# Kernel optimization log

Measured on AMD Instinct MI355X. Metric: run time of the kernel, lower is better.

## Reference

```python
import jax, jax.numpy as jnp
import numpy as np

B, CTX, QST, E, H = 8, 4096, 512, 300, 128

def setup_inputs() -> dict:
    key = jax.random.key(0)
    k1, k2, k3, k4 = jax.random.split(key, 4)
    context_sequence = jax.random.normal(k1, (B, CTX, E), dtype=jnp.float32)
    question_sequence = jax.random.normal(k2, (B, QST, E), dtype=jnp.float32)
    question_mask = jnp.ones((B, QST), dtype=jnp.int32)
    # dense layer params (PyTorch Linear: y = x @ W.T + b)
    bound = 1.0 / np.sqrt(E)
    W = jax.random.uniform(k3, (H, E), minval=-bound, maxval=bound, dtype=jnp.float32)
    b = jax.random.uniform(k4, (H,), minval=-bound, maxval=bound, dtype=jnp.float32)
    return {"context_sequence": context_sequence, "question_sequence": question_sequence,
            "question_mask": question_mask, "W": W, "b": b}

def reference(context_sequence, question_sequence, question_mask, W, b):
    # ReLU(dense(x)) for both sequences
    ctx_logits = jax.nn.relu(jnp.einsum('bce,he->bch', context_sequence, W) + b)   # [B, CTX, H]
    qst_logits = jax.nn.relu(jnp.einsum('bqe,he->bqh', question_sequence, W) + b)  # [B, QST, H]
    scores = jnp.einsum('bch,bqh->bcq', ctx_logits, qst_logits)                    # [B, CTX, QST]
    scores = jnp.where(question_mask[:, None, :] == 0, -jnp.inf, scores)
    attn = jax.nn.softmax(scores, axis=-1)
    return jnp.einsum('bcq,bqh->bch', attn, qst_logits)                            # [B, CTX, H]
```

## Files before the change

### kernel.cpp

```cpp
#include <hip/hip_runtime.h>
#include <hip/hip_bf16.h>

#define BB   8
#define SCTX 4096
#define SQ   512
#define EE   300
#define HH   128
#define EP   320
#define CST  328
#define LOG2E 1.4426950408889634f

typedef short short8 __attribute__((ext_vector_type(8)));
typedef float f32x4  __attribute__((ext_vector_type(4)));

#define MFMA16(a, b, c) __builtin_amdgcn_mfma_f32_16x16x32_bf16((a), (b), (c), 0, 0, 0)

__device__ __forceinline__ short f2bf(float f) {
  unsigned u = __builtin_bit_cast(unsigned, f);
  u += 0x7fffu + ((u >> 16) & 1u);
  return (short)(u >> 16);
}

__global__ void k_wpad(const float* __restrict__ W, short* __restrict__ wpad) {
  const int h = blockIdx.x, k = threadIdx.x;
  float v = (k < EE) ? W[h * EE + k] : 0.0f;
  wpad[h * EP + k] = f2bf(v);
}

__global__ __launch_bounds__(256) void k_qlog(const float* __restrict__ qst,
                                              const short* __restrict__ wpad,
                                              const float* __restrict__ bias,
                                              short* __restrict__ ql,
                                              short* __restrict__ qlT) {
  const int b = blockIdx.y;
  const int m0 = blockIdx.x * 32;
  const int tid = threadIdx.x;
  const int w = tid >> 6, l = tid & 63, t = l & 15, quad = l >> 4;
  const int g = w >> 1, hf = w & 1;

  __shared__ __align__(16) short cst[32 * CST];

  const float4* cbase = (const float4*)(qst + (size_t)(b * SQ + m0) * EE);
#pragma unroll
  for (int j = 0; j < 10; ++j) {
    int i4 = tid + j * 256;
    if (i4 < 2400) {
      float4 v = cbase[i4];
      int row = i4 / 75, c4 = i4 - row * 75;
      short* dp = cst + row * CST + c4 * 4;
      dp[0] = f2bf(v.x); dp[1] = f2bf(v.y); dp[2] = f2bf(v.z); dp[3] = f2bf(v.w);
    }
  }
  for (int i = tid; i < 320; i += 256) {
    int row = i / 10, c = (i - row * 10) * 2;
    cst[row * CST + 300 + c] = 0;
    cst[row * CST + 301 + c] = 0;
  }
  __syncthreads();

  const short* arow = cst + (g * 16 + t) * CST;
  f32x4 acc[4] = {};
#pragma unroll
  for (int kk = 0; kk < 10; ++kk) {
    const int k = kk * 32 + quad * 8;
    short8 a = *(const short8*)(arow + k);
#pragma unroll
    for (int n = 0; n < 4; ++n) {
      short8 w8 = *(const short8*)(wpad + ((hf * 4 + n) * 16 + t) * EP + k);
      acc[n] = MFMA16(a, w8, acc[n]);
    }
  }
#pragma unroll
  for (int n = 0; n < 4; ++n) {
    const int h = (hf * 4 + n) * 16 + t;
    const float bv = bias[h];
#pragma unroll
    for (int r = 0; r < 4; ++r) {
      float v = fmaxf(acc[n][r] + bv, 0.0f);
      short s16 = f2bf(v);
      const int row = m0 + g * 16 + quad * 4 + r;
      ql[((size_t)b * SQ + row) * HH + h] = s16;
      qlT[((size_t)b * HH + h) * SQ + row] = s16;
    }
  }
}

__global__ __launch_bounds__(256, 2) void k_attn(const float* __restrict__ ctx,
                                                 const short* __restrict__ wpad,
                                                 const float* __restrict__ bias,
                                                 const int* __restrict__ mask,
                                                 const short* __restrict__ ql,
                                                 const short* __restrict__ qlT,
                                                 float* __restrict__ out) {
  const int b = blockIdx.y;
  const int m0 = blockIdx.x * 64;
  const int tid = threadIdx.x;
  const int w = tid >> 6, l = tid & 63, t = l & 15, quad = l >> 4;
  const int g = w >> 1, hf = w & 1;

  __shared__ __align__(16) short uq[17408];
  __shared__ __align__(16) short uc[8704];
  __shared__ float maskb[SQ];
  short* cst = uq;
  short* qch = uq;
  short* clt = uc;
  short* pbw = uc + w * 2176;

  for (int i = tid; i < SQ; i += 256)
    maskb[i] = mask[b * SQ + i] ? 0.0f : -1e30f;

  for (int i = 0; i < 2; ++i) {
    const float4* cbase = (const float4*)(ctx + ((size_t)b * SCTX + m0 + i * 32) * EE);
#pragma unroll
    for (int j = 0; j < 10; ++j) {
      int i4 = tid + j * 256;
      if (i4 < 2400) {
        float4 v = cbase[i4];
        int row = i4 / 75, c4 = i4 - row * 75;
        short* dp = cst + row * CST + c4 * 4;
        dp[0] = f2bf(v.x); dp[1] = f2bf(v.y); dp[2] = f2bf(v.z); dp[3] = f2bf(v.w);
      }
    }
    for (int k = tid; k < 320; k += 256) {
      int row = k / 10, c = (k - row * 10) * 2;
      cst[row * CST + 300 + c] = 0;
      cst[row * CST + 301 + c] = 0;
    }
    __syncthreads();
    const short* arow = cst + (g * 16 + t) * CST;
    f32x4 acc[4] = {};
#pragma unroll
    for (int kk = 0; kk < 10; ++kk) {
      const int k = kk * 32 + quad * 8;
      short8 a = *(const short8*)(arow + k);
#pragma unroll
      for (int n = 0; n < 4; ++n) {
        short8 w8 = *(const short8*)(wpad + ((hf * 4 + n) * 16 + t) * EP + k);
        acc[n] = MFMA16(a, w8, acc[n]);
      }
    }
#pragma unroll
    for (int n = 0; n < 4; ++n) {
      const int h = (hf * 4 + n) * 16 + t;
      const float bv = bias[h];
#pragma unroll
      for (int r = 0; r < 4; ++r) {
        float v = fmaxf(acc[n][r] + bv, 0.0f);
        clt[(i * 32 + g * 16 + quad * 4 + r) * 136 + h] = f2bf(v);
      }
    }
    __syncthreads();
  }

  short8 af[4];
#pragma unroll
  for (int kk = 0; kk < 4; ++kk)
    af[kk] = *(const short8*)&clt[(w * 16 + t) * 136 + kk * 32 + quad * 8];

  f32x4 s[32];
  const short8* qsrc = (const short8*)(ql + (size_t)b * SQ * HH);
  short8 ld[8];
#pragma unroll
  for (int j = 0; j < 8; ++j) ld[j] = qsrc[tid + j * 256];
#pragma unroll
  for (int c = 0; c < 4; ++c) {
    if (c) __syncthreads();
#pragma unroll
    for (int j = 0; j < 8; ++j) {
      int i = tid + j * 256;
      int row = i >> 4, c16 = i & 15;
      *(short8*)&qch[row * 136 + c16 * 8] = ld[j];
    }
    __syncthreads();
    if (c < 3) {
#pragma unroll
      for (int j = 0; j < 8; ++j) ld[j] = qsrc[(c + 1) * 2048 + tid + j * 256];
    }
#pragma unroll
    for (int n2 = 0; n2 < 8; ++n2) {
      f32x4 sv = {0.f, 0.f, 0.f, 0.f};
      const short* qrow = qch + (n2 * 16 + t) * 136;
#pragma unroll
      for (int kk = 0; kk < 4; ++kk) {
        short8 b8 = *(const short8*)(qrow + kk * 32 + quad * 8);
        sv = MFMA16(af[kk], b8, sv);
      }
      s[c * 8 + n2] = sv;
    }
  }

#pragma unroll
  for (int n = 0; n < 32; ++n) {
    const float mb = maskb[(n >> 3) * 128 + (n & 7) * 16 + t];
    s[n][0] += mb; s[n][1] += mb; s[n][2] += mb; s[n][3] += mb;
  }
  f32x4 rmax = s[0];
#pragma unroll
  for (int n = 1; n < 32; ++n)
#pragma unroll
    for (int r = 0; r < 4; ++r) rmax[r] = fmaxf(rmax[r], s[n][r]);
#pragma unroll
  for (int off = 8; off; off >>= 1)
#pragma unroll
    for (int r = 0; r < 4; ++r) rmax[r] = fmaxf(rmax[r], __shfl_xor(rmax[r], off));
  f32x4 rsum = {0.f, 0.f, 0.f, 0.f};
#pragma unroll
  for (int n = 0; n < 32; ++n)
#pragma unroll
    for (int r = 0; r < 4; ++r) {
      float p = exp2f((s[n][r] - rmax[r]) * LOG2E);
      s[n][r] = p;
      rsum[r] += p;
    }
#pragma unroll
  for (int off = 8; off; off >>= 1)
#pragma unroll
    for (int r = 0; r < 4; ++r) rsum[r] += __shfl_xor(rsum[r], off);

  const short8* vsrc = (const short8*)(qlT + (size_t)b * HH * SQ);
#pragma unroll
  for (int j = 0; j < 8; ++j) {
    int i = tid + j * 256;
    ld[j] = vsrc[(i >> 4) * 64 + (i & 15)];
  }
  f32x4 o[8] = {};
#pragma unroll
  for (int c = 0; c < 4; ++c) {
    __syncthreads();
#pragma unroll
    for (int j = 0; j < 8; ++j) {
      int i = tid + j * 256;
      int row = i >> 4, c16 = i & 15;
      *(short8*)&qch[row * 136 + c16 * 8] = ld[j];
    }
#pragma unroll
    for (int n2 = 0; n2 < 8; ++n2)
#pragma unroll
      for (int r = 0; r < 4; ++r)
        pbw[(quad * 4 + r) * 136 + n2 * 16 + t] = f2bf(s[c * 8 + n2][r]);
    __syncthreads();
    if (c < 3) {
#pragma unroll
      for (int j = 0; j < 8; ++j) {
        int i = tid + j * 256;
        ld[j] = vsrc[(i >> 4) * 64 + (c + 1) * 16 + (i & 15)];
      }
    }
#pragma unroll
    for (int kk = 0; kk < 4; ++kk) {
      short8 pa = *(const short8*)&pbw[t * 136 + kk * 32 + quad * 8];
#pragma unroll
      for (int n = 0; n < 8; ++n) {
        short8 v8 = *(const short8*)&qch[(n * 16 + t) * 136 + kk * 32 + quad * 8];
        o[n] = MFMA16(pa, v8, o[n]);
      }
    }
  }

  f32x4 rinv;
#pragma unroll
  for (int r = 0; r < 4; ++r) rinv[r] = 1.0f / rsum[r];
  float* obase = out + ((size_t)b * SCTX + m0 + w * 16) * HH;
#pragma unroll
  for (int n = 0; n < 8; ++n)
#pragma unroll
    for (int r = 0; r < 4; ++r)
      obase[(quad * 4 + r) * HH + n * 16 + t] = o[n][r] * rinv[r];
}

extern "C" void kernel_launch(void* const* d_in, const int* in_sizes, int n_in,
                              void* d_out, int out_size, void* d_ws, size_t ws_size,
                              hipStream_t stream) {
  const float* ctx  = (const float*)d_in[0];
  const float* qst  = (const float*)d_in[1];
  const int*   mask = (const int*)d_in[2];
  const float* W    = (const float*)d_in[3];
  const float* bias = (const float*)d_in[4];
  float* out = (float*)d_out;

  short* wpad = (short*)d_ws;
  short* ql   = (short*)((char*)d_ws + 81920);
  short* qlT  = ql + (size_t)BB * SQ * HH;

  k_wpad<<<dim3(HH), dim3(EP), 0, stream>>>(W, wpad);
  k_qlog<<<dim3(SQ / 32, BB), dim3(256), 0, stream>>>(qst, wpad, bias, ql, qlT);
  k_attn<<<dim3(SCTX / 64, BB), dim3(256), 0, stream>>>(ctx, wpad, bias, mask, ql, qlT, out);
}
```

Before: 130.5 us.

## Use online softmax per chunk, swizzle W for coalesced MFMA loads, raise occupancy

The attention kernel now keeps a running max and sum per chunk of 128 questions instead of holding all 32 score tiles in registers, so register pressure drops and launch bounds go to 3 blocks per SU. The weight matrix is pre-swizzled into MFMA fragment order, so each lane reads a contiguous 16 bytes. The register prefetch of the next Q/V chunk is removed, which exposes global load latency at each chunk. It also adds a rescale of the output accumulators per chunk.

```diff
diff --git a/kernel.cpp b/kernel.cpp
--- a/kernel.cpp
+++ b/kernel.cpp
@@ -21,14 +21,15 @@
   return (short)(u >> 16);
 }
 
-__global__ void k_wpad(const float* __restrict__ W, short* __restrict__ wpad) {
+__global__ void k_wpad(const float* __restrict__ W, short* __restrict__ wsw) {
   const int h = blockIdx.x, k = threadIdx.x;
   float v = (k < EE) ? W[h * EE + k] : 0.0f;
-  wpad[h * EP + k] = f2bf(v);
+  const int m = h >> 4, t = h & 15, kk = k >> 5, quad = (k >> 3) & 3, j = k & 7;
+  wsw[((kk * 8 + m) * 64 + quad * 16 + t) * 8 + j] = f2bf(v);
 }
 
 __global__ __launch_bounds__(256) void k_qlog(const float* __restrict__ qst,
-                                              const short* __restrict__ wpad,
+                                              const short* __restrict__ wsw,
                                               const float* __restrict__ bias,
                                               short* __restrict__ ql,
                                               short* __restrict__ qlT) {
@@ -66,7 +67,7 @@
     short8 a = *(const short8*)(arow + k);
 #pragma unroll
     for (int n = 0; n < 4; ++n) {
-      short8 w8 = *(const short8*)(wpad + ((hf * 4 + n) * 16 + t) * EP + k);
+      short8 w8 = *(const short8*)(wsw + ((kk * 8 + hf * 4 + n) * 64 + l) * 8);
       acc[n] = MFMA16(a, w8, acc[n]);
     }
   }
@@ -85,8 +86,8 @@
   }
 }
 
-__global__ __launch_bounds__(256, 2) void k_attn(const float* __restrict__ ctx,
-                                                 const short* __restrict__ wpad,
+__global__ __launch_bounds__(256, 3) void k_attn(const float* __restrict__ ctx,
+                                                 const short* __restrict__ wsw,
                                                  const float* __restrict__ bias,
                                                  const int* __restrict__ mask,
                                                  const short* __restrict__ ql,
@@ -135,7 +136,7 @@
       short8 a = *(const short8*)(arow + k);
 #pragma unroll
       for (int n = 0; n < 4; ++n) {
-        short8 w8 = *(const short8*)(wpad + ((hf * 4 + n) * 16 + t) * EP + k);
+        short8 w8 = *(const short8*)(wsw + ((kk * 8 + hf * 4 + n) * 64 + l) * 8);
         acc[n] = MFMA16(a, w8, acc[n]);
       }
     }
@@ -157,25 +158,25 @@
   for (int kk = 0; kk < 4; ++kk)
     af[kk] = *(const short8*)&clt[(w * 16 + t) * 136 + kk * 32 + quad * 8];
 
-  f32x4 s[32];
   const short8* qsrc = (const short8*)(ql + (size_t)b * SQ * HH);
-  short8 ld[8];
-#pragma unroll
-  for (int j = 0; j < 8; ++j) ld[j] = qsrc[tid + j * 256];
-#pragma unroll
+  const short8* vsrc = (const short8*)(qlT + (size_t)b * HH * SQ);
+
+  f32x4 o[8] = {};
+  f32x4 m_run, l_run;
+#pragma unroll
+  for (int r = 0; r < 4; ++r) { m_run[r] = -3.0e38f; l_run[r] = 0.0f; }
+
   for (int c = 0; c < 4; ++c) {
     if (c) __syncthreads();
 #pragma unroll
     for (int j = 0; j < 8; ++j) {
       int i = tid + j * 256;
-      int row = i >> 4, c16 = i & 15;
-      *(short8*)&qch[row * 136 + c16 * 8] = ld[j];
-    }
-    __syncthreads();
-    if (c < 3) {
-#pragma unroll
-      for (int j = 0; j < 8; ++j) ld[j] = qsrc[(c + 1) * 2048 + tid + j * 256];
-    }
+      short8 v = qsrc[c * 2048 + i];
+      *(short8*)&qch[(i >> 4) * 136 + (i & 15) * 8] = v;
+    }
+    __syncthreads();
+
+    f32x4 s[8];
 #pragma unroll
     for (int n2 = 0; n2 < 8; ++n2) {
       f32x4 sv = {0.f, 0.f, 0.f, 0.f};
@@ -185,67 +186,61 @@
         short8 b8 = *(const short8*)(qrow + kk * 32 + quad * 8);
         sv = MFMA16(af[kk], b8, sv);
       }
-      s[c * 8 + n2] = sv;
-    }
-  }
-
-#pragma unroll
-  for (int n = 0; n < 32; ++n) {
-    const float mb = maskb[(n >> 3) * 128 + (n & 7) * 16 + t];
-    s[n][0] += mb; s[n][1] += mb; s[n][2] += mb; s[n][3] += mb;
-  }
-  f32x4 rmax = s[0];
-#pragma unroll
-  for (int n = 1; n < 32; ++n)
-#pragma unroll
-    for (int r = 0; r < 4; ++r) rmax[r] = fmaxf(rmax[r], s[n][r]);
-#pragma unroll
-  for (int off = 8; off; off >>= 1)
-#pragma unroll
-    for (int r = 0; r < 4; ++r) rmax[r] = fmaxf(rmax[r], __shfl_xor(rmax[r], off));
-  f32x4 rsum = {0.f, 0.f, 0.f, 0.f};
-#pragma unroll
-  for (int n = 0; n < 32; ++n)
+      const float mb = maskb[c * 128 + n2 * 16 + t];
+      sv[0] += mb; sv[1] += mb; sv[2] += mb; sv[3] += mb;
+      s[n2] = sv;
+    }
+
+    f32x4 cm = s[0];
+#pragma unroll
+    for (int n2 = 1; n2 < 8; ++n2)
+#pragma unroll
+      for (int r = 0; r < 4; ++r) cm[r] = fmaxf(cm[r], s[n2][r]);
+#pragma unroll
+    for (int off = 8; off; off >>= 1)
+#pragma unroll
+      for (int r = 0; r < 4; ++r) cm[r] = fmaxf(cm[r], __shfl_xor(cm[r], off));
+
+    f32x4 alpha, csum = {0.f, 0.f, 0.f, 0.f};
 #pragma unroll
     for (int r = 0; r < 4; ++r) {
-      float p = exp2f((s[n][r] - rmax[r]) * LOG2E);
-      s[n][r] = p;
-      rsum[r] += p;
-    }
-#pragma unroll
-  for (int off = 8; off; off >>= 1)
-#pragma unroll
-    for (int r = 0; r < 4; ++r) rsum[r] += __shfl_xor(rsum[r], off);
-
-  const short8* vsrc = (const short8*)(qlT + (size_t)b * HH * SQ);
-#pragma unroll
-  for (int j = 0; j < 8; ++j) {
-    int i = tid + j * 256;
-    ld[j] = vsrc[(i >> 4) * 64 + (i & 15)];
-  }
-  f32x4 o[8] = {};
-#pragma unroll
-  for (int c = 0; c < 4; ++c) {
+      float nm = fmaxf(m_run[r], cm[r]);
+      alpha[r] = exp2f((m_run[r] - nm) * LOG2E);
+      m_run[r] = nm;
+    }
+#pragma unroll
+    for (int n2 = 0; n2 < 8; ++n2)
+#pragma unroll
+      for (int r = 0; r < 4; ++r) {
+        float p = exp2f((s[n2][r] - m_run[r]) * LOG2E);
+        s[n2][r] = p;
+        csum[r] += p;
+      }
+#pragma unroll
+    for (int off = 8; off; off >>= 1)
+#pragma unroll
+      for (int r = 0; r < 4; ++r) csum[r] += __shfl_xor(csum[r], off);
+#pragma unroll
+    for (int r = 0; r < 4; ++r) l_run[r] = l_run[r] * alpha[r] + csum[r];
+#pragma unroll
+    for (int n = 0; n < 8; ++n)
+#pragma unroll
+      for (int r = 0; r < 4; ++r) o[n][r] *= alpha[r];
+
     __syncthreads();
 #pragma unroll
     for (int j = 0; j < 8; ++j) {
       int i = tid + j * 256;
-      int row = i >> 4, c16 = i & 15;
-      *(short8*)&qch[row * 136 + c16 * 8] = ld[j];
+      short8 v = vsrc[(i >> 4) * 64 + c * 16 + (i & 15)];
+      *(short8*)&qch[(i >> 4) * 136 + (i & 15) * 8] = v;
     }
 #pragma unroll
     for (int n2 = 0; n2 < 8; ++n2)
 #pragma unroll
       for (int r = 0; r < 4; ++r)
-        pbw[(quad * 4 + r) * 136 + n2 * 16 + t] = f2bf(s[c * 8 + n2][r]);
-    __syncthreads();
-    if (c < 3) {
-#pragma unroll
-      for (int j = 0; j < 8; ++j) {
-        int i = tid + j * 256;
-        ld[j] = vsrc[(i >> 4) * 64 + (c + 1) * 16 + (i & 15)];
-      }
-    }
+        pbw[(quad * 4 + r) * 136 + n2 * 16 + t] = f2bf(s[n2][r]);
+    __syncthreads();
+
 #pragma unroll
     for (int kk = 0; kk < 4; ++kk) {
       short8 pa = *(const short8*)&pbw[t * 136 + kk * 32 + quad * 8];
@@ -259,7 +254,7 @@
 
   f32x4 rinv;
 #pragma unroll
-  for (int r = 0; r < 4; ++r) rinv[r] = 1.0f / rsum[r];
+  for (int r = 0; r < 4; ++r) rinv[r] = 1.0f / l_run[r];
   float* obase = out + ((size_t)b * SCTX + m0 + w * 16) * HH;
 #pragma unroll
   for (int n = 0; n < 8; ++n)
@@ -278,11 +273,11 @@
   const float* bias = (const float*)d_in[4];
   float* out = (float*)d_out;
 
-  short* wpad = (short*)d_ws;
+  short* wsw  = (short*)d_ws;
   short* ql   = (short*)((char*)d_ws + 81920);
   short* qlT  = ql + (size_t)BB * SQ * HH;
 
-  k_wpad<<<dim3(HH), dim3(EP), 0, stream>>>(W, wpad);
-  k_qlog<<<dim3(SQ / 32, BB), dim3(256), 0, stream>>>(qst, wpad, bias, ql, qlT);
-  k_attn<<<dim3(SCTX / 64, BB), dim3(256), 0, stream>>>(ctx, wpad, bias, mask, ql, qlT, out);
-}
+  k_wpad<<<dim3(HH), dim3(EP), 0, stream>>>(W, wsw);
+  k_qlog<<<dim3(SQ / 32, BB), dim3(256), 0, stream>>>(qst, wsw, bias, ql, qlT);
+  k_attn<<<dim3(SCTX / 64, BB), dim3(256), 0, stream>>>(ctx, wsw, bias, mask, ql, qlT, out);
+}
```

New measurement: 147.4 us. 12.9% more time.
